# Kernel optimization log

Measured on AMD Instinct MI355X. Metric: run time of the kernel, lower is better.

## Reference

```python
import jax, jax.numpy as jnp
import numpy as np

BATCH = 32
NUM_PRIORS = 8732
NUM_CLASSES = 81          # includes background class 0
CENTER_VAR = 0.1
SIZE_VAR = 0.2
CONF_THR = 0.01
NMS_THR = 0.45
TOPK = 100                # per-class NMS candidates
MAX_DET = 100             # max detections per image


def setup_inputs() -> dict:
    key = jax.random.key(0)
    k1, k2, k3 = jax.random.split(key, 3)
    cls_logits = jax.random.normal(k1, (BATCH, NUM_PRIORS, NUM_CLASSES), jnp.float32)
    bbox_pred = jax.random.normal(k2, (BATCH, NUM_PRIORS, 4), jnp.float32)
    # center-form priors (cx, cy, w, h) in (0, 1)
    priors = jax.random.uniform(k3, (NUM_PRIORS, 4), jnp.float32, 0.05, 0.95)
    return {"cls_logits": cls_logits, "bbox_pred": bbox_pred, "priors": priors}


def _decode(loc, priors):
    # convert_locations_to_boxes (center form) then center_form_to_corner_form
    cxcy = loc[..., :2] * CENTER_VAR * priors[..., 2:] + priors[..., :2]
    wh = jnp.exp(loc[..., 2:] * SIZE_VAR) * priors[..., 2:]
    return jnp.concatenate([cxcy - wh * 0.5, cxcy + wh * 0.5], axis=-1)  # [.., 4] xyxy


def _pairwise_iou(b):
    # b: [K, 4] corner form
    lt = jnp.maximum(b[:, None, :2], b[None, :, :2])
    rb = jnp.minimum(b[:, None, 2:], b[None, :, 2:])
    wh = jnp.clip(rb - lt, 0.0)
    inter = wh[..., 0] * wh[..., 1]
    area = jnp.clip(b[:, 2] - b[:, 0], 0.0) * jnp.clip(b[:, 3] - b[:, 1], 0.0)
    return inter / (area[:, None] + area[None, :] - inter + 1e-9)


def _per_class_nms(scores_n, boxes_n):
    # scores_n: [N], boxes_n: [N, 4]
    s, idx = jax.lax.top_k(scores_n, TOPK)
    b = boxes_n[idx]                                # [K, 4]
    iou = _pairwise_iou(b)                          # [K, K]
    init = s > CONF_THR
    rng = jnp.arange(TOPK)

    def body(i, keep):
        sup = (iou[i] > NMS_THR) & keep[i] & (rng > i)
        return keep & ~sup

    keep = jax.lax.fori_loop(0, TOPK, body, init)   # greedy NMS on sorted boxes
    return jnp.where(keep, s, 0.0), b


def reference(cls_logits, bbox_pred, priors):
    scores = jax.nn.softmax(cls_logits, axis=-1)            # [B, N, C]
    boxes = _decode(bbox_pred, priors)                      # [B, N, 4]
    cls_scores = jnp.swapaxes(scores[..., 1:], 1, 2)        # [B, C-1, N] skip background
    nms_fn = jax.vmap(jax.vmap(_per_class_nms, in_axes=(0, None)), in_axes=(0, 0))
    s_k, b_k = nms_fn(cls_scores, boxes)                    # [B, C-1, K], [B, C-1, K, 4]
    labels = jnp.broadcast_to(jnp.arange(1, NUM_CLASSES)[None, :, None], s_k.shape)
    B = s_k.shape[0]
    flat = (NUM_CLASSES - 1) * TOPK
    s_f = s_k.reshape(B, flat)
    b_f = b_k.reshape(B, flat, 4)
    l_f = labels.reshape(B, flat)
    top_s, top_i = jax.lax.top_k(s_f, MAX_DET)              # keep best MAX_DET per image
    top_b = jnp.take_along_axis(b_f, top_i[..., None], axis=1)
    top_l = jnp.take_along_axis(l_f, top_i, axis=1)
    return top_b, top_s, top_l.astype(jnp.int32)
```

## Files before the change

### kernel.cpp

```cpp
#include <hip/hip_runtime.h>
#include <hip/hip_bf16.h>
#include <float.h>

#define BATCH    32
#define NPRIORS  8732
#define NT       137
#define NPAD     (NT * 64)
#define NV4T     (NPAD / 4)
#define NCLASSES 81
#define NC1      80
#define TOPK     100
#define MAXDET   100
#define FLATC    (NC1 * TOPK)
#define FV4      2000
#define NCAND    512
#define NBIN     1024
#define BINOFF   3040

__global__ __launch_bounds__(256) void softmax_transpose_kernel(
    const float* __restrict__ logits, float* __restrict__ scores_t) {
  int b = blockIdx.x / NT;
  int tile = blockIdx.x - b * NT;
  int n0 = tile * 64;
  int rows = min(64, NPRIORS - n0);

  int t = threadIdx.x;
  int r = t >> 2;
  int q = t & 3;

  __shared__ __align__(16) float lds[NC1 * 80];

  const bool live = (r < rows);

  float v[21];
  float s = 0.f;
  if (live) {
    const float* rowp = logits + ((size_t)b * NPRIORS + n0 + r) * NCLASSES;
#pragma unroll
    for (int k = 0; k < 20; ++k) v[k] = rowp[q + (k << 2)];
    v[20] = (q == 0) ? rowp[80] : -FLT_MAX;

    float m = -FLT_MAX;
#pragma unroll
    for (int k = 0; k < 20; ++k) m = fmaxf(m, v[k]);
    if (q == 0) m = fmaxf(m, v[20]);
    m = fmaxf(m, __shfl_xor(m, 1));
    m = fmaxf(m, __shfl_xor(m, 2));

#pragma unroll
    for (int k = 0; k < 20; ++k) {
      v[k] = expf(v[k] - m);
      s += v[k];
    }
    if (q == 0) {
      v[20] = expf(v[20] - m);
      s += v[20];
    }
    s += __shfl_xor(s, 1);
    s += __shfl_xor(s, 2);

#pragma unroll
    for (int k = 0; k < 20; ++k) {
      int c = q + (k << 2);
      if (c >= 1) lds[(c - 1) * 80 + r] = v[k] / s;
    }
    if (q == 0) lds[79 * 80 + r] = v[20] / s;
  } else {
#pragma unroll
    for (int k = 0; k < 20; ++k) {
      int c = q + (k << 2);
      if (c >= 1) lds[(c - 1) * 80 + r] = 0.f;
    }
    if (q == 0) lds[79 * 80 + r] = 0.f;
  }
  __syncthreads();

  float4* d4 = (float4*)(scores_t + (size_t)(b * NT + tile) * (NC1 * 64));
#pragma unroll
  for (int i = 0; i < 5; ++i) {
    int o4 = t + (i << 8);
    int c = o4 >> 4;
    int j = o4 & 15;
    d4[o4] = *(const float4*)&lds[c * 80 + (j << 2)];
  }
}

__device__ __forceinline__ float4 decode_box(float4 l, float4 p) {
  float cx = l.x * 0.1f * p.z + p.x;
  float cy = l.y * 0.1f * p.w + p.y;
  float w  = expf(l.z * 0.2f) * p.z;
  float h  = expf(l.w * 0.2f) * p.w;
  return make_float4(cx - w * 0.5f, cy - h * 0.5f, cx + w * 0.5f,
                     cy + h * 0.5f);
}

__device__ __forceinline__ unsigned long long cex(unsigned long long key,
                                                  unsigned long long p,
                                                  bool up, bool low) {
  return (up == low) ? (key < p ? key : p) : (key > p ? key : p);
}

__global__ __launch_bounds__(256, 8) void topk_nms_kernel(
    const float* __restrict__ scores_t, const float* __restrict__ loc,
    const float* __restrict__ priors, float* __restrict__ s_k,
    float* __restrict__ b_k) {
  const int bc = blockIdx.x;
  const int b = bc / NC1;
  const int c = bc - b * NC1;
  const int t = threadIdx.x;
  const int lane = t & 63;
  const int w = t >> 6;

  __shared__ __align__(16) unsigned int hist[NBIN * 2];
  __shared__ __align__(16) unsigned long long cand[NCAND];
  __shared__ __align__(16) unsigned long long skey[TOPK];
  __shared__ int s_cnt, s_cut, wtot[4];

  const float4* s4 = (const float4*)scores_t;
  const size_t base4 = (size_t)b * (NT * NC1 * 16) + (size_t)c * 16;

  float va[36];
#pragma unroll
  for (int i = 0; i < 9; ++i) {
    int p = t + (i << 8);
    float4 v = make_float4(0.f, 0.f, 0.f, 0.f);
    if (p < NV4T) v = s4[base4 + (size_t)(p >> 4) * (NC1 * 16) + (p & 15)];
    va[4 * i + 0] = v.x; va[4 * i + 1] = v.y;
    va[4 * i + 2] = v.z; va[4 * i + 3] = v.w;
  }
#pragma unroll
  for (int j = 0; j < 36; ++j) asm volatile("" : "+v"(va[j]));

  uint4* h4 = (uint4*)hist;
  const uint4 z4 = make_uint4(0u, 0u, 0u, 0u);
  h4[t] = z4;
  h4[t + 256] = z4;
  cand[t] = ~0ull;
  cand[t + 256] = ~0ull;
  if (t == 0) { s_cnt = 0; s_cut = 0; }
  __syncthreads();

#pragma unroll
  for (int j = 0; j < 36; ++j) {
    unsigned int bits = __float_as_uint(va[j]);
    if (bits != 0u) {
      int bin = (int)(bits >> 18) - BINOFF;
      bin = max(0, min(NBIN - 1, bin));
      atomicAdd(&hist[(bin << 1) | (lane & 1)], 1u);
    }
  }
  __syncthreads();

  int h[4];
  int ls;
  {
    uint4 a = h4[2 * t];
    uint4 b2 = h4[2 * t + 1];
    h[0] = (int)(a.x + a.y);
    h[1] = (int)(a.z + a.w);
    h[2] = (int)(b2.x + b2.y);
    h[3] = (int)(b2.z + b2.w);
    ls = h[0] + h[1] + h[2] + h[3];
  }
  int s = ls;
#pragma unroll
  for (int off = 1; off < 64; off <<= 1) {
    int o = __shfl_down(s, off);
    if (lane + off < 64) s += o;
  }
  if (lane == 0) wtot[w] = s;
  __syncthreads();
  int upper = 0;
  for (int w2 = w + 1; w2 < 4; ++w2) upper += wtot[w2];
  int run = (s - ls) + upper;
  int cutbin = -1;
#pragma unroll
  for (int k = 3; k >= 0; --k) {
    if (run < TOPK && run + h[k] >= TOPK) cutbin = (t << 2) + k;
    run += h[k];
  }
  if (cutbin >= 0) s_cut = cutbin;
  __syncthreads();

  const unsigned int cutbits = (unsigned int)(s_cut + BINOFF) << 18;

  unsigned long long msk = 0ull;
  int cnt = 0;
#pragma unroll
  for (int j = 0; j < 36; ++j) {
    unsigned int bits = __float_as_uint(va[j]);
    if (bits >= cutbits) { msk |= 1ull << j; ++cnt; }
  }
  int inc = cnt;
#pragma unroll
  for (int off = 1; off < 64; off <<= 1) {
    int o = __shfl_up(inc, off);
    if (lane >= off) inc += o;
  }
  int wtotal = __shfl(inc, 63);
  int wbase = 0;
  if (lane == 63) wbase = atomicAdd(&s_cnt, wtotal);
  wbase = __shfl(wbase, 63);
  int pos = wbase + inc - cnt;
#pragma unroll
  for (int j = 0; j < 36; ++j) {
    if ((msk >> j) & 1ull) {
      if (pos < NCAND) {
        unsigned int bits = __float_as_uint(va[j]);
        int idx = ((t + ((j >> 2) << 8)) << 2) + (j & 3);
        cand[pos] = (((unsigned long long)(~bits)) << 32) | (unsigned int)idx;
      }
      ++pos;
    }
  }
  __syncthreads();

  const int ncand = s_cnt;
  if (ncand <= 256) {
    unsigned long long key = cand[t];
#pragma unroll
    for (int k2 = 2; k2 <= 256; k2 <<= 1) {
#pragma unroll
      for (int j = 128; j > 0; j >>= 1) {
        if (j >= k2) continue;
        const bool up = ((t & k2) == 0);
        if (j >= 64) {
          cand[t] = key;
          __syncthreads();
          unsigned long long p = cand[t ^ j];
          key = cex(key, p, up, (t & j) == 0);
          __syncthreads();
        } else {
          unsigned long long p = __shfl_xor(key, j);
          key = cex(key, p, up, (lane & j) == 0);
        }
      }
    }
    if (t < TOPK) skey[t] = key;
  } else {
    int NS = 512;
    for (int k2 = 2; k2 <= NS; k2 <<= 1) {
      for (int j = k2 >> 1; j > 0; j >>= 1) {
        if (j >= 128) {
          __syncthreads();
          for (int p = t; p < NS; p += 256) {
            int ixj = p ^ j;
            if (ixj > p) {
              unsigned long long a = cand[p], c2 = cand[ixj];
              bool up = ((p & k2) == 0);
              if (up ? (a > c2) : (a < c2)) { cand[p] = c2; cand[ixj] = a; }
            }
          }
          __syncthreads();
        } else {
          int base = w << 7;
          if (base < NS) {
#pragma unroll
            for (int half = 0; half < 2; ++half) {
              int p = base + lane + (half << 6);
              int ixj = p ^ j;
              if (ixj > p) {
                unsigned long long a = cand[p], c2 = cand[ixj];
                bool up = ((p & k2) == 0);
                if (up ? (a > c2) : (a < c2)) { cand[p] = c2; cand[ixj] = a; }
              }
            }
          }
        }
      }
    }
    __syncthreads();
    if (t < TOPK) skey[t] = cand[t];
  }
  __syncthreads();

  typedef unsigned long long ull;
  float4* lbox  = (float4*)cand;
  float*  larea = (float*)((char*)cand + 1600);
  float*  lscore= (float*)((char*)cand + 2000);
  ull*    pmbuf = (ull*)hist;
  ull*    keepw = (ull*)((char*)hist + 6144);

  if (t < TOPK) {
    ull key2 = skey[t];
    float sv = __uint_as_float(~(unsigned int)(key2 >> 32));
    int idx = (int)(key2 & 0xFFFFFFFFull);
    if ((unsigned)idx >= NPRIORS) { idx = 0; sv = 0.f; }
    float4 bx = decode_box(((const float4*)loc)[(size_t)b * NPRIORS + idx],
                           ((const float4*)priors)[idx]);
    lbox[t] = bx;
    larea[t] = fmaxf(bx.z - bx.x, 0.f) * fmaxf(bx.w - bx.y, 0.f);
    lscore[t] = sv;
  }
  __syncthreads();

  const bool hasb = (lane + 64) < TOPK;
  float4 ba = lbox[lane];
  float aa = larea[lane];
  float4 bb2 = lbox[hasb ? (lane + 64) : 0];
  float ab = larea[hasb ? (lane + 64) : 0];

  ull ra0 = 0, ra1 = 0, rb1 = 0;
  int jlo = max(1, w * 25);
  int jhi = min(TOPK, w * 25 + 25);
  for (int j = jlo; j < jhi; ++j) {
    float4 bj = lbox[j];
    float aj = larea[j];
    if (lane < j) {
      float iw = fmaxf(fminf(ba.z, bj.z) - fmaxf(ba.x, bj.x), 0.f);
      float ih = fmaxf(fminf(ba.w, bj.w) - fmaxf(ba.y, bj.y), 0.f);
      float inter = iw * ih;
      float iou = inter / (aa + aj - inter + 1e-9f);
      if (iou > 0.45f) {
        if (j < 64) ra0 |= 1ull << j; else ra1 |= 1ull << (j - 64);
      }
    }
    if (hasb && (lane + 64) < j) {
      float iw = fmaxf(fminf(bb2.z, bj.z) - fmaxf(bb2.x, bj.x), 0.f);
      float ih = fmaxf(fminf(bb2.w, bj.w) - fmaxf(bb2.y, bj.y), 0.f);
      float inter = iw * ih;
      float iou = inter / (ab + aj - inter + 1e-9f);
      if (iou > 0.45f) rb1 |= 1ull << (j - 64);
    }
  }
  pmbuf[((w << 6) + lane) * 3 + 0] = ra0;
  pmbuf[((w << 6) + lane) * 3 + 1] = ra1;
  pmbuf[((w << 6) + lane) * 3 + 2] = rb1;
  __syncthreads();

  if (w == 0) {
    ull fa0 = pmbuf[lane * 3 + 0] | pmbuf[(64 + lane) * 3 + 0] |
              pmbuf[(128 + lane) * 3 + 0] | pmbuf[(192 + lane) * 3 + 0];
    ull fa1 = pmbuf[lane * 3 + 1] | pmbuf[(64 + lane) * 3 + 1] |
              pmbuf[(128 + lane) * 3 + 1] | pmbuf[(192 + lane) * 3 + 1];
    ull fb1 = pmbuf[lane * 3 + 2] | pmbuf[(64 + lane) * 3 + 2] |
              pmbuf[(128 + lane) * 3 + 2] | pmbuf[(192 + lane) * 3 + 2];

    float sva = lscore[lane];
    float svb = hasb ? lscore[lane + 64] : 0.f;
    ull keep0 = __ballot(sva > 0.01f);
    ull keep1 = __ballot(hasb && (svb > 0.01f));
    for (int i = 0; i < TOPK; ++i) {
      bool il = i < 64;
      bool kb = il ? ((keep0 >> i) & 1ull) : ((keep1 >> (i - 64)) & 1ull);
      ull m0 = __shfl(il ? fa0 : 0ull, i & 63);
      ull m1 = __shfl(il ? fa1 : fb1, i & 63);
      if (kb) { keep0 &= ~m0; keep1 &= ~m1; }
    }
    if (lane == 0) { keepw[0] = keep0; keepw[1] = keep1; }
  }
  __syncthreads();

  if (t < TOPK) {
    bool kp = (t < 64) ? ((keepw[0] >> t) & 1ull)
                       : ((keepw[1] >> (t - 64)) & 1ull);
    s_k[(size_t)bc * TOPK + t] = kp ? lscore[t] : 0.f;
    ((float4*)(b_k + (size_t)bc * TOPK * 4))[t] = lbox[t];
  }
}

__global__ __launch_bounds__(256) void final_topk_kernel(
    const float* __restrict__ s_k, const float* __restrict__ b_k,
    float* __restrict__ out) {
  const int b = blockIdx.x;
  const int t = threadIdx.x;
  const int lane = t & 63;
  const int w = t >> 6;

  __shared__ __align__(16) unsigned int hist[NBIN * 2];
  __shared__ __align__(16) unsigned long long cand[NCAND];
  __shared__ int s_cnt, s_cut, wtot[4];

  const float4* src4 = (const float4*)(s_k + (size_t)b * FLATC);

  float va[32];
#pragma unroll
  for (int i = 0; i < 8; ++i) {
    int p = t + (i << 8);
    float4 v = make_float4(0.f, 0.f, 0.f, 0.f);
    if (p < FV4) v = src4[p];
    va[4 * i + 0] = v.x; va[4 * i + 1] = v.y;
    va[4 * i + 2] = v.z; va[4 * i + 3] = v.w;
  }

  uint4* h4 = (uint4*)hist;
  const uint4 z4 = make_uint4(0u, 0u, 0u, 0u);
  h4[t] = z4;
  h4[t + 256] = z4;
  cand[t] = ~0ull;
  cand[t + 256] = ~0ull;
  if (t == 0) { s_cnt = 0; s_cut = 0; }
  __syncthreads();

#pragma unroll
  for (int j = 0; j < 32; ++j) {
    unsigned int bits = __float_as_uint(va[j]);
    if (bits != 0u) {
      int bin = (int)(bits >> 18) - BINOFF;
      bin = max(0, min(NBIN - 1, bin));
      atomicAdd(&hist[(bin << 1) | (lane & 1)], 1u);
    }
  }
  __syncthreads();

  int h[4];
  int ls;
  {
    uint4 a = h4[2 * t];
    uint4 b2 = h4[2 * t + 1];
    h[0] = (int)(a.x + a.y);
    h[1] = (int)(a.z + a.w);
    h[2] = (int)(b2.x + b2.y);
    h[3] = (int)(b2.z + b2.w);
    ls = h[0] + h[1] + h[2] + h[3];
  }
  int s = ls;
#pragma unroll
  for (int off = 1; off < 64; off <<= 1) {
    int o = __shfl_down(s, off);
    if (lane + off < 64) s += o;
  }
  if (lane == 0) wtot[w] = s;
  __syncthreads();
  int upper = 0;
  for (int w2 = w + 1; w2 < 4; ++w2) upper += wtot[w2];
  int run = (s - ls) + upper;
  int cutbin = -1;
#pragma unroll
  for (int k = 3; k >= 0; --k) {
    if (run < TOPK && run + h[k] >= TOPK) cutbin = (t << 2) + k;
    run += h[k];
  }
  if (cutbin >= 0) s_cut = cutbin;
  __syncthreads();

  const unsigned int cutbits = (unsigned int)(s_cut + BINOFF) << 18;

  unsigned int msk = 0u;
  int cnt = 0;
#pragma unroll
  for (int j = 0; j < 32; ++j) {
    unsigned int bits = __float_as_uint(va[j]);
    if (bits >= cutbits) { msk |= 1u << j; ++cnt; }
  }
  int inc = cnt;
#pragma unroll
  for (int off = 1; off < 64; off <<= 1) {
    int o = __shfl_up(inc, off);
    if (lane >= off) inc += o;
  }
  int wtotal = __shfl(inc, 63);
  int wbase = 0;
  if (lane == 63) wbase = atomicAdd(&s_cnt, wtotal);
  wbase = __shfl(wbase, 63);
  int pos = wbase + inc - cnt;
#pragma unroll
  for (int j = 0; j < 32; ++j) {
    if ((msk >> j) & 1u) {
      if (pos < NCAND) {
        unsigned int bits = __float_as_uint(va[j]);
        int idx = ((t + ((j >> 2) << 8)) << 2) + (j & 3);
        cand[pos] = (((unsigned long long)(~bits)) << 32) | (unsigned int)idx;
      }
      ++pos;
    }
  }
  __syncthreads();

  const int ncand = s_cnt;
  unsigned long long okey;
  if (ncand <= 256) {
    unsigned long long key = cand[t];
#pragma unroll
    for (int k2 = 2; k2 <= 256; k2 <<= 1) {
#pragma unroll
      for (int j = 128; j > 0; j >>= 1) {
        if (j >= k2) continue;
        const bool up = ((t & k2) == 0);
        if (j >= 64) {
          cand[t] = key;
          __syncthreads();
          unsigned long long p = cand[t ^ j];
          key = cex(key, p, up, (t & j) == 0);
          __syncthreads();
        } else {
          unsigned long long p = __shfl_xor(key, j);
          key = cex(key, p, up, (lane & j) == 0);
        }
      }
    }
    okey = key;
  } else {
    int NS = 512;
    for (int k2 = 2; k2 <= NS; k2 <<= 1) {
      for (int j = k2 >> 1; j > 0; j >>= 1) {
        if (j >= 128) {
          __syncthreads();
          for (int p = t; p < NS; p += 256) {
            int ixj = p ^ j;
            if (ixj > p) {
              unsigned long long a = cand[p], c2 = cand[ixj];
              bool up = ((p & k2) == 0);
              if (up ? (a > c2) : (a < c2)) { cand[p] = c2; cand[ixj] = a; }
            }
          }
          __syncthreads();
        } else {
          int base = w << 7;
          if (base < NS) {
#pragma unroll
            for (int half = 0; half < 2; ++half) {
              int p = base + lane + (half << 6);
              int ixj = p ^ j;
              if (ixj > p) {
                unsigned long long a = cand[p], c2 = cand[ixj];
                bool up = ((p & k2) == 0);
                if (up ? (a > c2) : (a < c2)) { cand[p] = c2; cand[ixj] = a; }
              }
            }
          }
        }
      }
    }
    __syncthreads();
    okey = cand[min(t, NCAND - 1)];
  }

  if (t < MAXDET) {
    unsigned long long key = okey;
    unsigned int vb = ~(unsigned int)(key >> 32);
    float sv = __uint_as_float(vb);
    int f = (int)(key & 0xFFFFFFFFull);
    if ((unsigned)f >= FLATC) { f = 0; sv = 0.f; }
    float4 bb = *(const float4*)(b_k + ((size_t)b * FLATC + f) * 4);
    ((float4*)out)[b * MAXDET + t] = bb;
    out[BATCH * MAXDET * 4 + b * MAXDET + t] = sv;
    int cls = f / TOPK + 1;
    out[BATCH * MAXDET * 5 + b * MAXDET + t] = (float)cls;
  }
}

extern "C" void kernel_launch(void* const* d_in, const int* in_sizes, int n_in,
                              void* d_out, int out_size, void* d_ws,
                              size_t ws_size, hipStream_t stream) {
  const float* cls_logits = (const float*)d_in[0];
  const float* bbox_pred  = (const float*)d_in[1];
  const float* priors     = (const float*)d_in[2];
  float* out = (float*)d_out;

  float* scores_t = (float*)d_ws;
  float* s_k = scores_t + (size_t)BATCH * NT * NC1 * 64;
  float* b_k = s_k + (size_t)BATCH * NC1 * TOPK;

  softmax_transpose_kernel<<<BATCH * NT, 256, 0, stream>>>(cls_logits,
                                                           scores_t);
  topk_nms_kernel<<<BATCH * NC1, 256, 0, stream>>>(scores_t, bbox_pred,
                                                   priors, s_k, b_k);
  final_topk_kernel<<<BATCH, 256, 0, stream>>>(s_k, b_k, out);
}
```

Measured before the change: 100.8 us.

## Fuse final per-image top-k into NMS kernel via last-block counter

Removes the separate final_topk kernel launch. Each per-class NMS block increments a per-image atomic counter, and the last block to finish for an image does the final top-100 selection over all class results. The counter is reset inside the softmax kernel. This saves one launch and its dependency gap, at the cost of threadfence/atomic synchronisation, a serialized tail on the last block, and rereading s_k twice from global memory instead of holding it in registers.

```diff
diff --git a/kernel.cpp b/kernel.cpp
--- a/kernel.cpp
+++ b/kernel.cpp
@@ -18,7 +18,10 @@
 #define BINOFF   3040
 
 __global__ __launch_bounds__(256) void softmax_transpose_kernel(
-    const float* __restrict__ logits, float* __restrict__ scores_t) {
+    const float* __restrict__ logits, float* __restrict__ scores_t,
+    unsigned int* __restrict__ done) {
+  if (blockIdx.x < BATCH && threadIdx.x == 0) done[blockIdx.x] = 0u;
+
   int b = blockIdx.x / NT;
   int tile = blockIdx.x - b * NT;
   int n0 = tile * 64;
@@ -103,7 +106,8 @@
 __global__ __launch_bounds__(256, 8) void topk_nms_kernel(
     const float* __restrict__ scores_t, const float* __restrict__ loc,
     const float* __restrict__ priors, float* __restrict__ s_k,
-    float* __restrict__ b_k) {
+    float* __restrict__ b_k, float* __restrict__ out,
+    unsigned int* __restrict__ done) {
   const int bc = blockIdx.x;
   const int b = bc / NC1;
   const int c = bc - b * NC1;
@@ -114,7 +118,7 @@
   __shared__ __align__(16) unsigned int hist[NBIN * 2];
   __shared__ __align__(16) unsigned long long cand[NCAND];
   __shared__ __align__(16) unsigned long long skey[TOPK];
-  __shared__ int s_cnt, s_cut, wtot[4];
+  __shared__ int s_cnt, s_cut, wtot[4], s_last;
 
   const float4* s4 = (const float4*)scores_t;
   const size_t base4 = (size_t)b * (NT * NC1 * 16) + (size_t)c * 16;
@@ -357,160 +361,134 @@
     s_k[(size_t)bc * TOPK + t] = kp ? lscore[t] : 0.f;
     ((float4*)(b_k + (size_t)bc * TOPK * 4))[t] = lbox[t];
   }
-}
-
-__global__ __launch_bounds__(256) void final_topk_kernel(
-    const float* __restrict__ s_k, const float* __restrict__ b_k,
-    float* __restrict__ out) {
-  const int b = blockIdx.x;
-  const int t = threadIdx.x;
-  const int lane = t & 63;
-  const int w = t >> 6;
-
-  __shared__ __align__(16) unsigned int hist[NBIN * 2];
-  __shared__ __align__(16) unsigned long long cand[NCAND];
-  __shared__ int s_cnt, s_cut, wtot[4];
-
-  const float4* src4 = (const float4*)(s_k + (size_t)b * FLATC);
-
-  float va[32];
-#pragma unroll
-  for (int i = 0; i < 8; ++i) {
-    int p = t + (i << 8);
-    float4 v = make_float4(0.f, 0.f, 0.f, 0.f);
-    if (p < FV4) v = src4[p];
-    va[4 * i + 0] = v.x; va[4 * i + 1] = v.y;
-    va[4 * i + 2] = v.z; va[4 * i + 3] = v.w;
-  }
-
-  uint4* h4 = (uint4*)hist;
-  const uint4 z4 = make_uint4(0u, 0u, 0u, 0u);
-  h4[t] = z4;
-  h4[t + 256] = z4;
-  cand[t] = ~0ull;
-  cand[t + 256] = ~0ull;
-  if (t == 0) { s_cnt = 0; s_cut = 0; }
-  __syncthreads();
-
-#pragma unroll
-  for (int j = 0; j < 32; ++j) {
-    unsigned int bits = __float_as_uint(va[j]);
-    if (bits != 0u) {
-      int bin = (int)(bits >> 18) - BINOFF;
-      bin = max(0, min(NBIN - 1, bin));
-      atomicAdd(&hist[(bin << 1) | (lane & 1)], 1u);
-    }
-  }
-  __syncthreads();
-
-  int h[4];
-  int ls;
+
+  __syncthreads();
+  if (t == 0) {
+    __threadfence();
+    s_last = (int)(atomicAdd(&done[b], 1u) == (unsigned)(NC1 - 1));
+  }
+  __syncthreads();
+  if (!s_last) return;
+  if (t == 0) __threadfence();
+  __syncthreads();
+
   {
-    uint4 a = h4[2 * t];
-    uint4 b2 = h4[2 * t + 1];
-    h[0] = (int)(a.x + a.y);
-    h[1] = (int)(a.z + a.w);
-    h[2] = (int)(b2.x + b2.y);
-    h[3] = (int)(b2.z + b2.w);
-    ls = h[0] + h[1] + h[2] + h[3];
-  }
-  int s = ls;
-#pragma unroll
-  for (int off = 1; off < 64; off <<= 1) {
-    int o = __shfl_down(s, off);
-    if (lane + off < 64) s += o;
-  }
-  if (lane == 0) wtot[w] = s;
-  __syncthreads();
-  int upper = 0;
-  for (int w2 = w + 1; w2 < 4; ++w2) upper += wtot[w2];
-  int run = (s - ls) + upper;
-  int cutbin = -1;
-#pragma unroll
-  for (int k = 3; k >= 0; --k) {
-    if (run < TOPK && run + h[k] >= TOPK) cutbin = (t << 2) + k;
-    run += h[k];
-  }
-  if (cutbin >= 0) s_cut = cutbin;
-  __syncthreads();
-
-  const unsigned int cutbits = (unsigned int)(s_cut + BINOFF) << 18;
-
-  unsigned int msk = 0u;
-  int cnt = 0;
-#pragma unroll
-  for (int j = 0; j < 32; ++j) {
-    unsigned int bits = __float_as_uint(va[j]);
-    if (bits >= cutbits) { msk |= 1u << j; ++cnt; }
-  }
-  int inc = cnt;
-#pragma unroll
-  for (int off = 1; off < 64; off <<= 1) {
-    int o = __shfl_up(inc, off);
-    if (lane >= off) inc += o;
-  }
-  int wtotal = __shfl(inc, 63);
-  int wbase = 0;
-  if (lane == 63) wbase = atomicAdd(&s_cnt, wtotal);
-  wbase = __shfl(wbase, 63);
-  int pos = wbase + inc - cnt;
-#pragma unroll
-  for (int j = 0; j < 32; ++j) {
-    if ((msk >> j) & 1u) {
-      if (pos < NCAND) {
-        unsigned int bits = __float_as_uint(va[j]);
-        int idx = ((t + ((j >> 2) << 8)) << 2) + (j & 3);
-        cand[pos] = (((unsigned long long)(~bits)) << 32) | (unsigned int)idx;
-      }
-      ++pos;
-    }
-  }
-  __syncthreads();
-
-  const int ncand = s_cnt;
-  unsigned long long okey;
-  if (ncand <= 256) {
-    unsigned long long key = cand[t];
-#pragma unroll
-    for (int k2 = 2; k2 <= 256; k2 <<= 1) {
-#pragma unroll
-      for (int j = 128; j > 0; j >>= 1) {
-        if (j >= k2) continue;
-        const bool up = ((t & k2) == 0);
-        if (j >= 64) {
-          cand[t] = key;
-          __syncthreads();
-          unsigned long long p = cand[t ^ j];
-          key = cex(key, p, up, (t & j) == 0);
-          __syncthreads();
-        } else {
-          unsigned long long p = __shfl_xor(key, j);
-          key = cex(key, p, up, (lane & j) == 0);
+    const float4* src4 = (const float4*)(s_k + (size_t)b * FLATC);
+
+    h4[t] = z4;
+    h4[t + 256] = z4;
+    cand[t] = ~0ull;
+    cand[t + 256] = ~0ull;
+    if (t == 0) { s_cnt = 0; s_cut = 0; }
+    __syncthreads();
+
+    for (int i = 0; i < 8; ++i) {
+      int p = t + (i << 8);
+      if (p < FV4) {
+        float4 v = src4[p];
+        float vv[4] = {v.x, v.y, v.z, v.w};
+#pragma unroll
+        for (int cc2 = 0; cc2 < 4; ++cc2) {
+          unsigned int bits = __float_as_uint(vv[cc2]);
+          if (bits != 0u) {
+            int bin = (int)(bits >> 18) - BINOFF;
+            bin = max(0, min(NBIN - 1, bin));
+            atomicAdd(&hist[(bin << 1) | (lane & 1)], 1u);
+          }
         }
       }
     }
-    okey = key;
-  } else {
-    int NS = 512;
-    for (int k2 = 2; k2 <= NS; k2 <<= 1) {
-      for (int j = k2 >> 1; j > 0; j >>= 1) {
-        if (j >= 128) {
-          __syncthreads();
-          for (int p = t; p < NS; p += 256) {
-            int ixj = p ^ j;
-            if (ixj > p) {
-              unsigned long long a = cand[p], c2 = cand[ixj];
-              bool up = ((p & k2) == 0);
-              if (up ? (a > c2) : (a < c2)) { cand[p] = c2; cand[ixj] = a; }
-            }
+    __syncthreads();
+
+    int h2[4];
+    int ls2;
+    {
+      uint4 a = h4[2 * t];
+      uint4 b2 = h4[2 * t + 1];
+      h2[0] = (int)(a.x + a.y);
+      h2[1] = (int)(a.z + a.w);
+      h2[2] = (int)(b2.x + b2.y);
+      h2[3] = (int)(b2.z + b2.w);
+      ls2 = h2[0] + h2[1] + h2[2] + h2[3];
+    }
+    int s2 = ls2;
+#pragma unroll
+    for (int off = 1; off < 64; off <<= 1) {
+      int o = __shfl_down(s2, off);
+      if (lane + off < 64) s2 += o;
+    }
+    if (lane == 0) wtot[w] = s2;
+    __syncthreads();
+    int upper2 = 0;
+    for (int w2 = w + 1; w2 < 4; ++w2) upper2 += wtot[w2];
+    int run2 = (s2 - ls2) + upper2;
+    int cutbin2 = -1;
+#pragma unroll
+    for (int k = 3; k >= 0; --k) {
+      if (run2 < TOPK && run2 + h2[k] >= TOPK) cutbin2 = (t << 2) + k;
+      run2 += h2[k];
+    }
+    if (cutbin2 >= 0) s_cut = cutbin2;
+    __syncthreads();
+
+    const unsigned int cutb4 = (unsigned int)(s_cut + BINOFF) << 18;
+
+    for (int i = 0; i < 8; ++i) {
+      int p = t + (i << 8);
+      bool inb = (p < FV4);
+      float4 v = make_float4(0.f, 0.f, 0.f, 0.f);
+      if (inb) v = src4[p];
+      float vv[4] = {v.x, v.y, v.z, v.w};
+#pragma unroll
+      for (int cc2 = 0; cc2 < 4; ++cc2) {
+        unsigned int bits = __float_as_uint(vv[cc2]);
+        bool pred = inb && (bits >= cutb4);
+        unsigned long long mB = __ballot(pred);
+        if (mB) {
+          int base = 0;
+          if (lane == 0) base = atomicAdd(&s_cnt, (int)__popcll(mB));
+          base = __shfl(base, 0);
+          if (pred) {
+            int pos2 = base + (int)__popcll(mB & ((1ull << lane) - 1ull));
+            if (pos2 < NCAND)
+              cand[pos2] = (((unsigned long long)(~bits)) << 32) |
+                           (unsigned int)((p << 2) + cc2);
           }
-          __syncthreads();
-        } else {
-          int base = w << 7;
-          if (base < NS) {
-#pragma unroll
-            for (int half = 0; half < 2; ++half) {
-              int p = base + lane + (half << 6);
+        }
+      }
+    }
+    __syncthreads();
+
+    const int nc4 = s_cnt;
+    unsigned long long okey;
+    if (nc4 <= 256) {
+      unsigned long long key = cand[t];
+#pragma unroll
+      for (int k2 = 2; k2 <= 256; k2 <<= 1) {
+#pragma unroll
+        for (int j = 128; j > 0; j >>= 1) {
+          if (j >= k2) continue;
+          const bool up = ((t & k2) == 0);
+          if (j >= 64) {
+            cand[t] = key;
+            __syncthreads();
+            unsigned long long p = cand[t ^ j];
+            key = cex(key, p, up, (t & j) == 0);
+            __syncthreads();
+          } else {
+            unsigned long long p = __shfl_xor(key, j);
+            key = cex(key, p, up, (lane & j) == 0);
+          }
+        }
+      }
+      okey = key;
+    } else {
+      int NS = 512;
+      for (int k2 = 2; k2 <= NS; k2 <<= 1) {
+        for (int j = k2 >> 1; j > 0; j >>= 1) {
+          if (j >= 128) {
+            __syncthreads();
+            for (int p = t; p < NS; p += 256) {
               int ixj = p ^ j;
               if (ixj > p) {
                 unsigned long long a = cand[p], c2 = cand[ixj];
@@ -518,25 +496,40 @@
                 if (up ? (a > c2) : (a < c2)) { cand[p] = c2; cand[ixj] = a; }
               }
             }
+            __syncthreads();
+          } else {
+            int base = w << 7;
+            if (base < NS) {
+#pragma unroll
+              for (int half = 0; half < 2; ++half) {
+                int p = base + lane + (half << 6);
+                int ixj = p ^ j;
+                if (ixj > p) {
+                  unsigned long long a = cand[p], c2 = cand[ixj];
+                  bool up = ((p & k2) == 0);
+                  if (up ? (a > c2) : (a < c2)) { cand[p] = c2; cand[ixj] = a; }
+                }
+              }
+            }
           }
         }
       }
-    }
-    __syncthreads();
-    okey = cand[min(t, NCAND - 1)];
-  }
-
-  if (t < MAXDET) {
-    unsigned long long key = okey;
-    unsigned int vb = ~(unsigned int)(key >> 32);
-    float sv = __uint_as_float(vb);
-    int f = (int)(key & 0xFFFFFFFFull);
-    if ((unsigned)f >= FLATC) { f = 0; sv = 0.f; }
-    float4 bb = *(const float4*)(b_k + ((size_t)b * FLATC + f) * 4);
-    ((float4*)out)[b * MAXDET + t] = bb;
-    out[BATCH * MAXDET * 4 + b * MAXDET + t] = sv;
-    int cls = f / TOPK + 1;
-    out[BATCH * MAXDET * 5 + b * MAXDET + t] = (float)cls;
+      __syncthreads();
+      okey = cand[min(t, NCAND - 1)];
+    }
+
+    if (t < MAXDET) {
+      unsigned long long key = okey;
+      unsigned int vb = ~(unsigned int)(key >> 32);
+      float sv = __uint_as_float(vb);
+      int f = (int)(key & 0xFFFFFFFFull);
+      if ((unsigned)f >= FLATC) { f = 0; sv = 0.f; }
+      float4 bb = *(const float4*)(b_k + ((size_t)b * FLATC + f) * 4);
+      ((float4*)out)[b * MAXDET + t] = bb;
+      out[BATCH * MAXDET * 4 + b * MAXDET + t] = sv;
+      int cls = f / TOPK + 1;
+      out[BATCH * MAXDET * 5 + b * MAXDET + t] = (float)cls;
+    }
   }
 }
 
@@ -551,10 +544,11 @@
   float* scores_t = (float*)d_ws;
   float* s_k = scores_t + (size_t)BATCH * NT * NC1 * 64;
   float* b_k = s_k + (size_t)BATCH * NC1 * TOPK;
+  unsigned int* done = (unsigned int*)(b_k + (size_t)BATCH * NC1 * TOPK * 4);
 
   softmax_transpose_kernel<<<BATCH * NT, 256, 0, stream>>>(cls_logits,
-                                                           scores_t);
+                                                           scores_t, done);
   topk_nms_kernel<<<BATCH * NC1, 256, 0, stream>>>(scores_t, bbox_pred,
-                                                   priors, s_k, b_k);
-  final_topk_kernel<<<BATCH, 256, 0, stream>>>(s_k, b_k, out);
+                                                   priors, s_k, b_k, out,
+                                                   done);
 }
```

Measured after the change: 167.7 us. 1.66x slower.
